# Kernel optimization log

Hardware: AMD Instinct MI355X
Metric: run time of the kernel (lower is better)

Reference implementation:

```python
import jax, jax.numpy as jnp
import numpy as np

KERNEL = 10   # kernel_size (asserted == 10 in the original)
HEADS = 4
BN_SCALE = 1.0 / np.sqrt(1.0 + 1e-5)  # eval-mode BatchNorm1d (running mean 0, var 1, affine 1/0)


def get_dct_matrix(N):
    k = np.arange(N)[:, None].astype(np.float64)
    i = np.arange(N)[None, :].astype(np.float64)
    w = np.full((N, 1), np.sqrt(2.0 / N))
    w[0, 0] = np.sqrt(1.0 / N)
    dct_m = w * np.cos(np.pi * (i + 0.5) * k / N)
    idct_m = np.linalg.inv(dct_m)
    return dct_m.astype(np.float32), idct_m.astype(np.float32)


def conv1d(x, w):  # x [B,C,L], w [O,I,K], valid, no bias
    return jax.lax.conv_general_dilated(x, w, (1,), 'VALID',
                                        dimension_numbers=('NCH', 'OIH', 'NCH'))


def conv_stack(x, w1, w2):  # Conv1d(k=6) -> ReLU -> Conv1d(k=5) -> ReLU
    return jax.nn.relu(conv1d(jax.nn.relu(conv1d(x, w1)), w2))


# vmap over the 4 heads' weights -> [H,B,D,L]
heads_conv = jax.vmap(conv_stack, in_axes=(None, 0, 0))


def _forward(src, cq1, cq2, ck1, ck2, lw, lb, giw, gia, gib, gbw, gba, gbb,
             gow, goa, gob, dct_n, output_n, input_n):
    bs, in_feat = src.shape[0], src.shape[2]
    src = src[:, :input_n]                                   # [B,50,48]
    src_key = jnp.swapaxes(src, 1, 2)[:, :, :input_n - output_n]  # [B,48,25]
    src_query = jnp.swapaxes(src, 1, 2)[:, :, -KERNEL:]           # [B,48,10]

    dct_np, idct_np = get_dct_matrix(KERNEL + output_n)
    dct_m = jnp.asarray(dct_np)
    idct_m = jnp.asarray(idct_np)

    vn = input_n - KERNEL - output_n + 1  # 16 overlapping value windows
    vl = KERNEL + output_n                # window length 35
    idx = np.arange(vl)[None, :] + np.arange(vn)[:, None]    # [16,35]
    windows = src[:, idx]                                    # [B,16,35,48]
    # DCT per window then flatten per-joint coeffs: [B,16,48*dct_n]
    val = jnp.einsum('dv,bnvf->bndf', dct_m[:dct_n], windows)
    src_value = jnp.swapaxes(val, 2, 3).reshape(bs, vn, -1)  # [B,16,480]

    key_h = heads_conv(src_key / 1000.0, ck1, ck2)           # [H,B,512,16]
    query_h = heads_conv(src_query / 1000.0, cq1, cq2)       # [H,B,512,1]

    # sum-normalized (non-softmax) attention
    score = jnp.einsum('hbdq,hbdk->hbqk', query_h, key_h) + 1e-15  # [H,B,1,16]
    att_w = score / jnp.sum(score, axis=3, keepdims=True)
    dct_att = jnp.einsum('hbk,bkf->hbf', att_w[:, :, 0], src_value)  # [H,B,480]
    dct_att = dct_att.reshape(HEADS, bs, in_feat, dct_n)
    att_cat = jnp.transpose(dct_att, (1, 0, 2, 3)).reshape(bs, HEADS * in_feat, dct_n)
    # Linear over the concatenated head/joint axis: [B,48,dct_n]
    att_lin = jnp.einsum('bmd,nm->bnd', att_cat, lw) + lb[None, :, None]

    # last kernel_size frames + last frame repeated output_n times
    gather_idx = np.concatenate([np.arange(input_n - KERNEL, input_n),
                                 np.full(output_n, input_n - 1)])
    input_gcn = src[:, gather_idx]                           # [B,35,48]
    dct_in = jnp.einsum('dv,bvf->bfd', dct_m[:dct_n], input_gcn)  # [B,48,10]
    dct_in = jnp.concatenate([dct_in, att_lin], axis=-1)     # [B,48,20]

    # GCN (Mao et al. style): learnable adjacency [48,48], eval-mode BN, tanh
    def gc(h, a, w, b):
        return jnp.einsum('nm,bmf->bnf', a, h @ w) + b

    y = jnp.tanh(gc(dct_in, gia, giw, gib) * BN_SCALE)       # [B,48,512]
    for s in range(gbw.shape[0]):
        r = y
        for j in range(2):
            y = jnp.tanh(gc(y, gba[s, j], gbw[s, j], gbb[s, j]) * BN_SCALE)
        y = y + r
    dct_out = gc(y, goa, gow, gob) + dct_in                  # [B,48,20]

    out_gcn = jnp.einsum('vd,bnd->bvn', idct_m[:, :dct_n], dct_out[:, :, :dct_n])  # [B,35,48]
    return out_gcn[:, :, None, :]                            # [B,35,itera=1,48]


def setup_inputs() -> dict:
    key = jax.random.key(0)
    ks = jax.random.split(key, 16)
    bs, in_feat, d_model, dct_n = 256, 48, 512, 10
    s = 0.05
    return {
        'src': jax.random.normal(ks[0], (bs, 50, in_feat), jnp.float32) * 1000.0,
        'convQ_w1': jax.random.normal(ks[1], (HEADS, d_model, in_feat, 6), jnp.float32) * s,
        'convQ_w2': jax.random.normal(ks[2], (HEADS, d_model, d_model, 5), jnp.float32) * s,
        'convK_w1': jax.random.normal(ks[3], (HEADS, d_model, in_feat, 6), jnp.float32) * s,
        'convK_w2': jax.random.normal(ks[4], (HEADS, d_model, d_model, 5), jnp.float32) * s,
        'linear_w': jax.random.normal(ks[5], (in_feat, HEADS * in_feat), jnp.float32) * s,
        'linear_b': jax.random.normal(ks[6], (in_feat,), jnp.float32) * s,
        'gc_in_w': jax.random.normal(ks[7], (2 * dct_n, d_model), jnp.float32) * s,
        'gc_in_att': jax.random.normal(ks[8], (in_feat, in_feat), jnp.float32) * s,
        'gc_in_b': jax.random.normal(ks[9], (d_model,), jnp.float32) * s,
        'gcb_w': jax.random.normal(ks[10], (2, 2, d_model, d_model), jnp.float32) * s,
        'gcb_att': jax.random.normal(ks[11], (2, 2, in_feat, in_feat), jnp.float32) * s,
        'gcb_b': jax.random.normal(ks[12], (2, 2, d_model), jnp.float32) * s,
        'gc_out_w': jax.random.normal(ks[13], (d_model, 2 * dct_n), jnp.float32) * s,
        'gc_out_att': jax.random.normal(ks[14], (in_feat, in_feat), jnp.float32) * s,
        'gc_out_b': jax.random.normal(ks[15], (2 * dct_n,), jnp.float32) * s,
        'dct_n': 10, 'output_n': 25, 'input_n': 50, 'itera': 1,
    }


def reference(src, convQ_w1, convQ_w2, convK_w1, convK_w2, linear_w, linear_b,
              gc_in_w, gc_in_att, gc_in_b, gcb_w, gcb_att, gcb_b,
              gc_out_w, gc_out_att, gc_out_b, dct_n, output_n, input_n, itera):
    # itera=1 path only (itera>1 in the original references undefined attrs)
    return _forward(src, convQ_w1, convQ_w2, convK_w1, convK_w2, linear_w, linear_b,
                    gc_in_w, gc_in_att, gc_in_b, gcb_w, gcb_att, gcb_b,
                    gc_out_w, gc_out_att, gc_out_b, dct_n, output_n, input_n)
```

## Files before the change

kernel.cpp:

```cpp
#include <hip/hip_runtime.h>
#include <math.h>

static constexpr float BN_SCALE_F = 0.9999950000374997f;

typedef __bf16 bf16;
typedef bf16 bf16x8 __attribute__((ext_vector_type(8)));
typedef bf16 bf16x4 __attribute__((ext_vector_type(4)));
typedef float floatx4 __attribute__((ext_vector_type(4)));

#define GLOBAL_AS __attribute__((address_space(1)))
#define LDS_AS __attribute__((address_space(3)))

enum { BM_SRC = 0, BM_R1K = 1, BM_PLAIN = 3 };

__device__ __forceinline__ float tanh_fast(float x) {
    const float e = __expf(2.f * x);
    return 1.f - 2.f / (e + 1.f);
}

__device__ __forceinline__ void d_trw1(int id, const float* w, bf16* wt) {
    if (id < 4 * 512 * 320) {
        int ho = id / 320, c = id % 320;
        float v = (c < 288) ? w[(long)ho * 288 + (c % 48) * 6 + (c / 48)] * 1e-3f : 0.f;
        wt[id] = (bf16)v;
    }
}
__global__ __launch_bounds__(256) void k_prep(
    const float* __restrict__ src, const float* __restrict__ cq1,
    const float* __restrict__ ck1, const float* __restrict__ cq2,
    const float* __restrict__ ck2, const float* __restrict__ gbw,
    const float* __restrict__ giw, const float* __restrict__ gow,
    const float* __restrict__ gba, float* __restrict__ dct10,
    bf16* __restrict__ srcbf, bf16* __restrict__ w1tq, bf16* __restrict__ w1tk,
    bf16* __restrict__ w2tq, bf16* __restrict__ w2tk, bf16* __restrict__ gbwF,
    bf16* __restrict__ giwF, bf16* __restrict__ gowT, bf16* __restrict__ gbaP) {
    __shared__ float lds[4160];
    int bb = blockIdx.x;
    const int t = threadIdx.x;
    if (bb < 2) {
        int id = bb * 256 + t;
        if (id < 350) {
            int k = id / 35, i = id % 35;
            double w = (k == 0) ? sqrt(1.0 / 35.0) : sqrt(2.0 / 35.0);
            dct10[id] = (float)(w * cos(3.14159265358979323846 * (i + 0.5) * k / 35.0));
        }
        return;
    }
    bb -= 2;
    if (bb < 2401) {
        int id = bb * 256 + t;
        if (id < 614656) srcbf[id] = (bf16)(id < 614400 ? src[id] : 0.f);
        return;
    }
    bb -= 2401;
    if (bb < 2560) { d_trw1(bb * 256 + t, cq1, w1tq); return; }
    bb -= 2560;
    if (bb < 2560) { d_trw1(bb * 256 + t, ck1, w1tk); return; }
    bb -= 2560;
    if (bb < 4096) {
        const bool isQ = bb < 2048;
        const int ho = isQ ? bb : bb - 2048;
        const float* wrow = (isQ ? cq2 : ck2) + (long)ho * 2560;
        bf16* orow = (isQ ? w2tq : w2tk) + (long)ho * 2560;
        for (int j = t; j < 2560; j += 256) lds[j] = wrow[j];
        __syncthreads();
        for (int c = t; c < 2560; c += 256) {
            const int k = c >> 9, ii = c & 511;
            orow[c] = (bf16)lds[ii * 5 + k];
        }
        return;
    }
    bb -= 4096;
    if (bb < 256) {
        const int l = bb >> 6, tile = bb & 63;
        const int tr = tile >> 3, tc = tile & 7;
        const float* in = gbw + (long)l * 262144;
        bf16* o = gbwF + (long)l * 262144;
#pragma unroll
        for (int r = 0; r < 16; ++r) {
            const int kl = (t >> 6) * 16 + r, ml = t & 63;
            lds[kl * 65 + ml] = in[(long)(tr * 64 + kl) * 512 + tc * 64 + ml];
        }
        __syncthreads();
        for (int j = t; j < 4096; j += 256) {
            const int q = j >> 9, r4 = j & 511;
            const int gl = q >> 2, sl = (q >> 1) & 1, jt = q & 1;
            const int lane = r4 >> 3, e = r4 & 7;
            const int fr = lane & 15, fq = lane >> 4;
            const int kk = sl * 32 + fq * 8 + e;
            const int ff = gl * 32 + jt * 16 + fr;
            o[(long)(tc * 2 + gl) * 16384 + (long)(tr * 2 + sl) * 1024 + jt * 512 + r4] =
                (bf16)lds[kk * 65 + ff];
        }
        return;
    }
    bb -= 256;
    if (bb < 128) {
        int id = bb * 256 + t;
        if (id < 32768) {
            const int r2 = id & 2047;
            const int s = r2 >> 10, r3 = r2 & 1023;
            const int jt = r3 >> 9, r4 = r3 & 511;
            const int lane = r4 >> 3, e = r4 & 7;
            const int fr = lane & 15, fq = lane >> 4;
            const int g = id >> 11;
            const int k = s * 32 + fq * 8 + e;
            const int f = g * 32 + jt * 16 + fr;
            giwF[id] = (bf16)(k < 20 ? giw[k * 512 + f] : 0.f);
        }
        return;
    }
    bb -= 128;
    if (bb < 64) {
        int id = bb * 256 + t;
        int d = id >> 9, k = id & 511;
        gowT[id] = (bf16)(d < 20 ? gow[k * 20 + d] : 0.f);
        return;
    }
    bb -= 64;
    {
        int id = bb * 256 + t;
        if (id < 12288) {
            int l = id / 3072, r = id % 3072, n = r >> 6, m = r & 63;
            gbaP[id] = (bf16)(m < 48 ? gba[l * 2304 + n * 48 + m] : 0.f);
        }
    }
}

struct GP {
    const bf16* A;
    const bf16* B;
    bf16* C;
    int NT;
    int toff;
    int nTiles;
    long aStr, bStr, cStr;
};
template <int BM1, int BM2>
__global__ __launch_bounds__(256) void mgemm2(GP p1, GP p2, const int splitX,
                                              const int M, const int K) {
    const bool first = (int)blockIdx.x < splitX;
    const GP p = first ? p1 : p2;
    const int bx = first ? (int)blockIdx.x : (int)blockIdx.x - splitX;
    if (bx >= p.nTiles) return;
    __shared__ bf16 As[128 * 64];
    __shared__ bf16 Bs[128 * 64];
    const int tid = threadIdx.x;
    const int wave = tid >> 6;
    const int lane = tid & 63;
    const int wm = (wave & 1) << 6;
    const int wn = (wave >> 1) << 6;
    const int m0 = blockIdx.y * 128;
    const int n0 = bx * 128;
    const bf16* A = p.A + (long)blockIdx.z * p.aStr;
    const bf16* B = p.B + (long)blockIdx.z * p.bStr;

    const int srow = lane >> 3;
    const int gch = (lane & 7) ^ srow;
    const bf16* aptr[4];
    const bf16* bptr[4];
#pragma unroll
    for (int i = 0; i < 4; ++i) {
        const int ar = wave * 32 + i * 8 + srow;
        aptr[i] = A + (long)(m0 + ar) * K + gch * 8;
        const int n = n0 + ar;
        long bbase;
        const bool isSrc = first ? (BM1 == BM_SRC) : (BM2 == BM_SRC);
        if (isSrc)
            bbase = (long)(n / p.NT) * 2400 + (long)((n % p.NT) + p.toff) * 48;
        else
            bbase = (long)n * K;
        bptr[i] = B + bbase + gch * 8;
    }
    const int ldsOff = wave * 32 * 64;

    floatx4 acc[4][4];
#pragma unroll
    for (int j = 0; j < 4; ++j)
#pragma unroll
        for (int i = 0; i < 4; ++i) acc[j][i] = (floatx4){0.f, 0.f, 0.f, 0.f};

    const int fr = lane & 15;
    const int fq = lane >> 4;
    const int fx = lane & 7;

    for (int k0 = 0; k0 < K; k0 += 64) {
#pragma unroll
        for (int i = 0; i < 4; ++i) {
            __builtin_amdgcn_global_load_lds(
                (const GLOBAL_AS void*)(aptr[i] + k0),
                (LDS_AS void*)(As + ldsOff + i * 512), 16, 0, 0);
            __builtin_amdgcn_global_load_lds(
                (const GLOBAL_AS void*)(bptr[i] + k0),
                (LDS_AS void*)(Bs + ldsOff + i * 512), 16, 0, 0);
        }
        __syncthreads();
#pragma unroll
        for (int kk = 0; kk < 2; ++kk) {
            bf16x8 af[4], bfr[4];
#pragma unroll
            for (int im = 0; im < 4; ++im)
                af[im] = *(const bf16x8*)(As + (wm + im * 16 + fr) * 64 +
                                          ((((kk << 2) + fq) ^ fx) << 3));
#pragma unroll
            for (int in = 0; in < 4; ++in)
                bfr[in] = *(const bf16x8*)(Bs + (wn + in * 16 + fr) * 64 +
                                           ((((kk << 2) + fq) ^ fx) << 3));
#pragma unroll
            for (int in = 0; in < 4; ++in)
#pragma unroll
                for (int im = 0; im < 4; ++im)
                    acc[in][im] = __builtin_amdgcn_mfma_f32_16x16x32_bf16(
                        af[im], bfr[in], acc[in][im], 0, 0, 0);
        }
        __syncthreads();
    }
#pragma unroll
    for (int in = 0; in < 4; ++in) {
        const long n = n0 + wn + in * 16 + fr;
#pragma unroll
        for (int im = 0; im < 4; ++im) {
            floatx4 v = acc[in][im];
            const long m = m0 + wm + im * 16 + (fq << 2);
            v.x = fmaxf(v.x, 0.f);
            v.y = fmaxf(v.y, 0.f);
            v.z = fmaxf(v.z, 0.f);
            v.w = fmaxf(v.w, 0.f);
            bf16* C = p.C + (long)blockIdx.z * p.cStr + n * M + m;
            bf16x4 ov;
            ov[0] = (bf16)v.x;
            ov[1] = (bf16)v.y;
            ov[2] = (bf16)v.z;
            ov[3] = (bf16)v.w;
            *(bf16x4*)C = ov;
        }
    }
}

__global__ __launch_bounds__(256) void k_conv2(
    const bf16* __restrict__ w2tk, const bf16* __restrict__ r1k,
    bf16* __restrict__ keyh, const bf16* __restrict__ w2tq,
    const bf16* __restrict__ r1q, bf16* __restrict__ qh) {
    const int K = 2560;
    int bx, by, bz;
    const bf16 *A, *B;
    bf16* C;
    bool r1kMode;
    long aStr, bStr, cStr;
    {
        const int i = blockIdx.x;
        if (i < 1024) {
            const int slot = i & 7;
            bz = slot >> 1;
            const int half = slot & 1;
            const int j = i >> 3;
            bx = half * 16 + (j & 15);
            by = j >> 4;
            A = w2tk; B = r1k; C = keyh; r1kMode = true;
            aStr = 512L * 2560; bStr = 2621440L; cStr = 2097152L;
        } else {
            const int j = i - 1024;
            bz = j >> 4;
            const int r = j & 15;
            bx = r & 1;
            by = r >> 1;
            A = w2tq; B = r1q; C = qh; r1kMode = false;
            aStr = 512L * 2560; bStr = 655360L; cStr = 131072L;
        }
    }
    __shared__ bf16 As[64 * 64];
    __shared__ bf16 Bs[128 * 64];
    const int tid = threadIdx.x;
    const int wave = tid >> 6;
    const int lane = tid & 63;
    const int wm = (wave & 1) * 32;
    const int wn = (wave >> 1) * 64;
    const int m0 = by * 64;
    const int n0 = bx * 128;
    A += (long)bz * aStr;
    B += (long)bz * bStr;

    const int srow = lane >> 3;
    const int gch = (lane & 7) ^ srow;
    const bf16* aptr[2];
    const bf16* bptr[4];
#pragma unroll
    for (int i = 0; i < 2; ++i) {
        const int ar = wave * 16 + i * 8 + srow;
        aptr[i] = A + (long)(m0 + ar) * K + gch * 8;
    }
#pragma unroll
    for (int i = 0; i < 4; ++i) {
        const int ar = wave * 32 + i * 8 + srow;
        const int n = n0 + ar;
        const long bbase = r1kMode ? (long)((n >> 4) * 20 + (n & 15)) * 512
                                   : (long)n * K;
        bptr[i] = B + bbase + gch * 8;
    }

    floatx4 acc[4][2];
#pragma unroll
    for (int j = 0; j < 4; ++j)
#pragma unroll
        for (int i = 0; i < 2; ++i) acc[j][i] = (floatx4){0.f, 0.f, 0.f, 0.f};

    const int fr = lane & 15;
    const int fq = lane >> 4;
    const int fx = lane & 7;

    for (int k0 = 0; k0 < K; k0 += 64) {
#pragma unroll
        for (int i = 0; i < 2; ++i)
            __builtin_amdgcn_global_load_lds(
                (const GLOBAL_AS void*)(aptr[i] + k0),
                (LDS_AS void*)(As + (wave * 16 + i * 8) * 64), 16, 0, 0);
#pragma unroll
        for (int i = 0; i < 4; ++i)
            __builtin_amdgcn_global_load_lds(
                (const GLOBAL_AS void*)(bptr[i] + k0),
                (LDS_AS void*)(Bs + (wave * 32 + i * 8) * 64), 16, 0, 0);
        __syncthreads();
#pragma unroll
        for (int kk = 0; kk < 2; ++kk) {
            bf16x8 af[2], bfr[4];
#pragma unroll
            for (int im = 0; im < 2; ++im)
                af[im] = *(const bf16x8*)(As + (wm + im * 16 + fr) * 64 +
                                          ((((kk << 2) + fq) ^ fx) << 3));
#pragma unroll
            for (int in = 0; in < 4; ++in)
                bfr[in] = *(const bf16x8*)(Bs + (wn + in * 16 + fr) * 64 +
                                           ((((kk << 2) + fq) ^ fx) << 3));
#pragma unroll
            for (int in = 0; in < 4; ++in)
#pragma unroll
                for (int im = 0; im < 2; ++im)
                    acc[in][im] = __builtin_amdgcn_mfma_f32_16x16x32_bf16(
                        af[im], bfr[in], acc[in][im], 0, 0, 0);
        }
        __syncthreads();
    }
#pragma unroll
    for (int in = 0; in < 4; ++in) {
        const long n = n0 + wn + in * 16 + fr;
#pragma unroll
        for (int im = 0; im < 2; ++im) {
            floatx4 v = acc[in][im];
            const long m = m0 + wm + im * 16 + (fq << 2);
            v.x = fmaxf(v.x, 0.f);
            v.y = fmaxf(v.y, 0.f);
            v.z = fmaxf(v.z, 0.f);
            v.w = fmaxf(v.w, 0.f);
            bf16* Cp = C + (long)bz * cStr + n * 512 + m;
            bf16x4 ov;
            ov[0] = (bf16)v.x;
            ov[1] = (bf16)v.y;
            ov[2] = (bf16)v.z;
            ov[3] = (bf16)v.w;
            *(bf16x4*)Cp = ov;
        }
    }
}

__global__ __launch_bounds__(512) void k_att(
    const bf16* __restrict__ qh, const bf16* __restrict__ keyh,
    const float* __restrict__ src, const float* __restrict__ dct10,
    const float* __restrict__ lw, const float* __restrict__ lb,
    const float* __restrict__ gia, float* __restrict__ dctin,
    bf16* __restrict__ z0) {
    const int b = blockIdx.x;
    const int t = threadIdx.x;
    __shared__ float BIG[9216];
    __shared__ float WD[2400];
    __shared__ float D[350];
    __shared__ float L[1920];
    __shared__ float dinS[960];
    __shared__ float sS[64];
    __shared__ float awS[64];

    {
        const int g = t >> 3, lane = t & 7;
        const int h = g >> 4, tt = g & 15;
        const bf16* q = qh + ((long)h * 256 + b) * 512 + lane * 64;
        const bf16* kr = keyh + (long)h * 2097152 + ((long)b * 16 + tt) * 512 + lane * 64;
        float p = 0.f;
#pragma unroll
        for (int i = 0; i < 8; ++i) {
            const bf16x8 qv = *(const bf16x8*)(q + i * 8);
            const bf16x8 kv = *(const bf16x8*)(kr + i * 8);
#pragma unroll
            for (int j = 0; j < 8; ++j) p = fmaf((float)qv[j], (float)kv[j], p);
        }
        p += __shfl_down(p, 4, 8);
        p += __shfl_down(p, 2, 8);
        p += __shfl_down(p, 1, 8);
        if (lane == 0) sS[g] = p + 1e-15f;
    }
    for (int i = t; i < 2400; i += 512) WD[i] = src[(long)b * 2400 + i];
    for (int i = t; i < 350; i += 512) D[i] = dct10[i];
    __syncthreads();
    if (t < 4) {
        float s = 0.f;
#pragma unroll
        for (int k = 0; k < 16; ++k) s += sS[t * 16 + k];
        const float inv = 1.f / s;
#pragma unroll
        for (int k = 0; k < 16; ++k) awS[t * 16 + k] = sS[t * 16 + k] * inv;
    }
    __syncthreads();
    if (t < 480) {
        const int f = t / 10, d = t % 10;
        float dreg[35];
#pragma unroll
        for (int v = 0; v < 35; ++v) dreg[v] = D[d * 35 + v];
#pragma unroll 2
        for (int n = 0; n < 16; ++n) {
            float acc = 0.f;
#pragma unroll
            for (int v = 0; v < 35; ++v)
                acc = fmaf(dreg[v], WD[(n + v) * 48 + f], acc);
            BIG[n * 480 + t] = acc;
        }
        float acc = 0.f;
#pragma unroll
        for (int v = 0; v < 10; ++v)
            acc = fmaf(dreg[v], WD[(40 + v) * 48 + f], acc);
        float cs = 0.f;
#pragma unroll
        for (int v = 10; v < 35; ++v) cs += dreg[v];
        acc = fmaf(cs, WD[49 * 48 + f], acc);
        dinS[f * 20 + d] = acc;
        dctin[(long)b * 960 + f * 20 + d] = acc;
    }
    __syncthreads();
    for (int p = 0; p < 4; ++p) {
        const int idx = t + p * 512;
        if (idx < 1920) {
            const int h = idx / 480, j = idx % 480;
            float acc = 0.f;
#pragma unroll
            for (int k = 0; k < 16; ++k)
                acc = fmaf(awS[h * 16 + k], BIG[k * 480 + j], acc);
            L[idx] = acc;
        }
    }
    __syncthreads();
    for (int i = t; i < 9216; i += 512) BIG[i] = lw[i];
    for (int i = t; i < 2304; i += 512) WD[i] = gia[i];
    __syncthreads();
    if (t < 480) {
        const int n = t / 10, d = t % 10;
        float acc = lb[n];
#pragma unroll
        for (int h = 0; h < 4; ++h)
#pragma unroll
            for (int f = 0; f < 48; ++f)
                acc = fmaf(BIG[n * 192 + h * 48 + f], L[h * 480 + f * 10 + d], acc);
        dinS[n * 20 + 10 + d] = acc;
        dctin[(long)b * 960 + n * 20 + 10 + d] = acc;
    }
    __syncthreads();
    for (int p = 0; p < 2; ++p) {
        const int idx = t + p * 512;
        if (idx < 960) {
            const int n = idx / 20, d = idx % 20;
            float acc = 0.f;
#pragma unroll
            for (int m = 0; m < 48; ++m)
                acc = fmaf(WD[n * 48 + m], dinS[m * 20 + d], acc);
            z0[((long)b * 48 + n) * 64 + d] = (bf16)acc;
        }
    }
    for (int i = t; i < 2112; i += 512) {
        const int n = i / 44, c = 20 + i % 44;
        z0[((long)b * 48 + n) * 64 + c] = (bf16)0.f;
    }
}

template <bool TOUT, int S>
__device__ __forceinline__ void gcn_matmul3(
    const bf16* __restrict__ zSrc, const bf16* __restrict__ Wf,
    const float* __restrict__ bias, const bf16* __restrict__ resT,
    bf16* __restrict__ outS, const int wave, const int lane) {
    const int fr = lane & 15, fq = lane >> 4;
    const int f0 = wave * 32;
    floatx4 acc[3][2];
#pragma unroll
    for (int it = 0; it < 3; ++it)
#pragma unroll
        for (int jt = 0; jt < 2; ++jt) acc[it][jt] = (floatx4){0.f, 0.f, 0.f, 0.f};
    const bf16* wp = Wf + (long)wave * (S * 1024) + (lane << 3);
    bf16x8 w0[4], w1[4];
    constexpr int PRE = (S < 3) ? S : 3;
#pragma unroll
    for (int s = 0; s < PRE; ++s) {
        w0[s] = *(const bf16x8*)(wp + s * 1024);
        w1[s] = *(const bf16x8*)(wp + s * 1024 + 512);
    }
#pragma unroll
    for (int s = 0; s < S; ++s) {
        bf16x8 af[3];
#pragma unroll
        for (int it = 0; it < 3; ++it)
            af[it] = *(const bf16x8*)(zSrc + (it * 16 + fr) * 520 + s * 32 + fq * 8);
        if (s + 3 < S) {
            const int ns = (s + 3) & 3;
            w0[ns] = *(const bf16x8*)(wp + (s + 3) * 1024);
            w1[ns] = *(const bf16x8*)(wp + (s + 3) * 1024 + 512);
        }
        const int sl = s & 3;
#pragma unroll
        for (int it = 0; it < 3; ++it) {
            acc[it][0] = __builtin_amdgcn_mfma_f32_16x16x32_bf16(af[it], w0[sl],
                                                                acc[it][0], 0, 0, 0);
            acc[it][1] = __builtin_amdgcn_mfma_f32_16x16x32_bf16(af[it], w1[sl],
                                                                acc[it][1], 0, 0, 0);
        }
    }
#pragma unroll
    for (int jt = 0; jt < 2; ++jt) {
        const int f = f0 + jt * 16 + fr;
        const float bv = bias[f];
#pragma unroll
        for (int it = 0; it < 3; ++it) {
            const int ir0 = it * 16 + fq * 4;
            float v[4];
#pragma unroll
            for (int r = 0; r < 4; ++r)
                v[r] = tanh_fast((acc[it][jt][r] + bv) * BN_SCALE_F);
            if (resT) {
                const bf16x4 rv = *(const bf16x4*)(resT + f * 48 + ir0);
#pragma unroll
                for (int r = 0; r < 4; ++r) v[r] += (float)rv[r];
            }
            if (TOUT) {
                bf16x4 ov;
#pragma unroll
                for (int r = 0; r < 4; ++r) ov[r] = (bf16)v[r];
                *(bf16x4*)(outS + f * 48 + ir0) = ov;
            } else {
#pragma unroll
                for (int r = 0; r < 4; ++r)
                    outS[(ir0 + r) * 520 + f] = (bf16)v[r];
            }
        }
    }
}

__device__ __forceinline__ void gcn_attmul2(const bf16* __restrict__ gA,
                                            const bf16* __restrict__ YinT,
                                            bf16* __restrict__ zOut,
                                            const int wave, const int lane) {
    const int fr = lane & 15, fq = lane >> 4;
    const int f0 = wave * 32;
    floatx4 acc[3][2];
#pragma unroll
    for (int it = 0; it < 3; ++it)
#pragma unroll
        for (int jt = 0; jt < 2; ++jt) acc[it][jt] = (floatx4){0.f, 0.f, 0.f, 0.f};
    bf16x8 af0[3], af1[3], bv0[2], bv1[2];
#pragma unroll
    for (int it = 0; it < 3; ++it) {
        af0[it] = *(const bf16x8*)(gA + (it * 16 + fr) * 64 + fq * 8);
        af1[it] = *(const bf16x8*)(gA + (it * 16 + fr) * 64 + 32 + fq * 8);
    }
#pragma unroll
    for (int jt = 0; jt < 2; ++jt) {
        const int f = f0 + jt * 16 + fr;
        bv0[jt] = *(const bf16x8*)(YinT + f * 48 + fq * 8);
        bv1[jt] = *(const bf16x8*)(YinT + f * 48 + 32 + fq * 8);
    }
#pragma unroll
    for (int it = 0; it < 3; ++it)
#pragma unroll
        for (int jt = 0; jt < 2; ++jt) {
            acc[it][jt] = __builtin_amdgcn_mfma_f32_16x16x32_bf16(af0[it], bv0[jt],
                                                                 acc[it][jt], 0, 0, 0);
            acc[it][jt] = __builtin_amdgcn_mfma_f32_16x16x32_bf16(af1[it], bv1[jt],
                                                                 acc[it][jt], 0, 0, 0);
        }
#pragma unroll
    for (int jt = 0; jt < 2; ++jt) {
        const int f = f0 + jt * 16 + fr;
#pragma unroll
        for (int it = 0; it < 3; ++it)
#pragma unroll
            for (int r = 0; r < 4; ++r)
                zOut[(it * 16 + fq * 4 + r) * 520 + f] = (bf16)acc[it][jt][r];
    }
}

__global__ __launch_bounds__(1024) void k_gcn(
    const bf16* __restrict__ z0, const bf16* __restrict__ giwF,
    const float* __restrict__ gib, const bf16* __restrict__ gbwF,
    const bf16* __restrict__ gbaP, const float* __restrict__ gbb,
    const float* __restrict__ goa, const bf16* __restrict__ gowT,
    const float* __restrict__ gob, const float* __restrict__ dctin,
    const float* __restrict__ dct10, float* __restrict__ out) {
    const int b = blockIdx.x;
    const int t = threadIdx.x;
    const int wave = t >> 6, lane = t & 63;
    __shared__ __align__(16) bf16 yaS[24976];
    __shared__ __align__(16) bf16 ybS[24592];
    __shared__ __align__(16) bf16 zS[48 * 520];

    if (t < 384) {
        const int r = t >> 3, c = t & 7;
        *(bf16x8*)(zS + r * 520 + c * 8) =
            *(const bf16x8*)(z0 + ((long)b * 48 + r) * 64 + c * 8);
    } else if (t < 400) {
        yaS[24576 + (t - 384)] = (bf16)0.f;
    } else if (t < 416) {
        ybS[24576 + (t - 400)] = (bf16)0.f;
    }
    __syncthreads();
    gcn_matmul3<true, 2>(zS, giwF, gib, nullptr, yaS, wave, lane);
    __syncthreads();

#pragma unroll
    for (int l = 0; l < 4; ++l) {
        const bf16* YinT = (l == 0 || l == 3) ? yaS : ybS;
        gcn_attmul2(gbaP + l * 3072, YinT, zS, wave, lane);
        __syncthreads();
        const bf16* Res = (l == 1) ? yaS : (l == 3 ? ybS : nullptr);
        if (l < 3)
            gcn_matmul3<true, 16>(zS, gbwF + (long)l * 262144, gbb + l * 512,
                                  Res, (l < 2) ? ybS : yaS, wave, lane);
        else
            gcn_matmul3<false, 16>(zS, gbwF + 3L * 262144, gbb + 3 * 512, Res,
                                   yaS, wave, lane);
        __syncthreads();
    }
    float* T2 = (float*)ybS;
    float* dS = ((float*)ybS) + 960;
    float* goaS = ((float*)ybS) + 1920;
    float* Df = ((float*)ybS) + 4224;
    if (t < 384) {
        const int fr2 = lane & 15, fq2 = lane >> 4;
        const int it = wave >> 1, jt = wave & 1;
        floatx4 accT = (floatx4){0.f, 0.f, 0.f, 0.f};
        const bf16* ap = yaS + (it * 16 + fr2) * 520 + fq2 * 8;
        const bf16* gp = gowT + (long)(jt * 16 + fr2) * 512 + fq2 * 8;
        for (int k0 = 0; k0 < 512; k0 += 32) {
            const bf16x8 av = *(const bf16x8*)(ap + k0);
            const bf16x8 gv = *(const bf16x8*)(gp + k0);
            accT = __builtin_amdgcn_mfma_f32_16x16x32_bf16(av, gv, accT, 0, 0, 0);
        }
        const int d = jt * 16 + fr2;
        if (d < 20) {
#pragma unroll
            for (int r = 0; r < 4; ++r) {
                const int m = it * 16 + fq2 * 4 + r;
                T2[m * 20 + d] = accT[r];
            }
        }
    } else {
        for (int i = t - 384; i < 2304; i += 640) goaS[i] = goa[i];
        for (int i = t - 384; i < 350; i += 640) Df[i] = dct10[i];
    }
    __syncthreads();
    if (t < 960) {
        const int n = t / 20, d = t % 20;
        float acc = gob[d] + dctin[(long)b * 960 + t];
#pragma unroll
        for (int m = 0; m < 48; ++m)
            acc = fmaf(goaS[n * 48 + m], T2[m * 20 + d], acc);
        dS[t] = acc;
    }
    __syncthreads();
    for (int e = t; e < 1680; e += 1024) {
        const int v = e / 48, n = e % 48;
        float acc = 0.f;
#pragma unroll
        for (int d = 0; d < 10; ++d)
            acc = fmaf(Df[d * 35 + v], dS[n * 20 + d], acc);
        out[(long)b * 1680 + e] = acc;
    }
}

static constexpr size_t WS_DCT10 = 0;
static constexpr size_t WS_ATTW = 1536;
static constexpr size_t WS_QH = WS_ATTW + 65536;
static constexpr size_t WS_DCTIN = WS_QH + 2097152;
static constexpr size_t WS_DCTOUT = WS_DCTIN + 983040;
static constexpr size_t WS_SRCVAL = WS_DCTOUT + 983040;
static constexpr size_t WS_PAD0 = WS_SRCVAL + 7864320;
static constexpr size_t WS_GOWT = WS_PAD0;
static constexpr size_t WS_GBAP = WS_PAD0 + 32768;
static constexpr size_t WS_SRCBF = WS_PAD0 + 8388608;
static constexpr size_t WS_W1TQ = WS_SRCBF + 1229824;
static constexpr size_t WS_W1TK = WS_W1TQ + 1310720;
static constexpr size_t WS_W2TQ = WS_W1TK + 1310720;
static constexpr size_t WS_W2TK = WS_W2TQ + 10485760;
static constexpr size_t WS_GBWT = WS_W2TK + 10485760;
static constexpr size_t WS_R1K = WS_GBWT + 2097152;
static constexpr size_t WS_R1Q = WS_R1K + 20971520;
static constexpr size_t WS_T = WS_R1Q + 5242880;
static constexpr size_t WS_GIWP = WS_T + 50331648;
static constexpr size_t WS_KEYH = WS_T;
static constexpr size_t WS_Z0 = WS_T + 17825792;

extern "C" void kernel_launch(void* const* d_in, const int* in_sizes, int n_in,
                              void* d_out, int out_size, void* d_ws,
                              size_t ws_size, hipStream_t stream) {
    const float* src = (const float*)d_in[0];
    const float* cq1 = (const float*)d_in[1];
    const float* cq2 = (const float*)d_in[2];
    const float* ck1 = (const float*)d_in[3];
    const float* ck2 = (const float*)d_in[4];
    const float* lw = (const float*)d_in[5];
    const float* lb = (const float*)d_in[6];
    const float* giw = (const float*)d_in[7];
    const float* gia = (const float*)d_in[8];
    const float* gib = (const float*)d_in[9];
    const float* gbw = (const float*)d_in[10];
    const float* gba = (const float*)d_in[11];
    const float* gbb = (const float*)d_in[12];
    const float* gow = (const float*)d_in[13];
    const float* goa = (const float*)d_in[14];
    const float* gob = (const float*)d_in[15];
    float* out = (float*)d_out;
    char* ws = (char*)d_ws;

    float* dct10 = (float*)(ws + WS_DCT10);
    bf16* qh = (bf16*)(ws + WS_QH);
    float* dctin = (float*)(ws + WS_DCTIN);
    bf16* keyh = (bf16*)(ws + WS_KEYH);
    bf16* srcbf = (bf16*)(ws + WS_SRCBF);
    bf16* w1tq = (bf16*)(ws + WS_W1TQ);
    bf16* w1tk = (bf16*)(ws + WS_W1TK);
    bf16* w2tq = (bf16*)(ws + WS_W2TQ);
    bf16* w2tk = (bf16*)(ws + WS_W2TK);
    bf16* gbwF = (bf16*)(ws + WS_GBWT);
    bf16* r1k = (bf16*)(ws + WS_R1K);
    bf16* r1q = (bf16*)(ws + WS_R1Q);
    bf16* giwF = (bf16*)(ws + WS_GIWP);
    bf16* gowT = (bf16*)(ws + WS_GOWT);
    bf16* gbaP = (bf16*)(ws + WS_GBAP);
    bf16* z0 = (bf16*)(ws + WS_Z0);

    k_prep<<<12115, 256, 0, stream>>>(src, cq1, ck1, cq2, ck2, gbw, giw, gow,
                                      gba, dct10, srcbf, w1tq, w1tk, w2tq,
                                      w2tk, gbwF, giwF, gowT, gbaP);

    {
        GP pk{w1tk, srcbf, r1k, 20, 0, 40, 512L * 320, 0L, 5120L * 512};
        GP pq{w1tq, srcbf, r1q, 5, 40, 10, 512L * 320, 0L, 1280L * 512};
        mgemm2<BM_SRC, BM_SRC><<<dim3(56, 4, 4), 256, 0, stream>>>(pk, pq, 40,
                                                                   512, 320);
    }
    k_conv2<<<1088, 256, 0, stream>>>(w2tk, r1k, keyh, w2tq, r1q, qh);

    k_att<<<256, 512, 0, stream>>>(qh, keyh, src, dct10, lw, lb, gia, dctin, z0);

    k_gcn<<<256, 1024, 0, stream>>>(z0, giwF, gib, gbwF, gbaP, gbb, goa, gowT,
                                    gob, dctin, dct10, out);
}
```

Before: 306.0 us.

## Pre-pack conv2 weights into MFMA fragment order and load A directly to registers

The prep kernel now writes the second conv weights in a fragment-major layout that matches the MFMA A-operand lane order. k_conv2 then reads A fragments straight from global memory into registers, with no LDS staging, and keeps only B in LDS. The wave tiling changes so each wave covers all 64 M rows and 32 N columns. This drops the A LDS traffic and its shared-memory footprint, in exchange for more register pressure and uncoalesced-latency exposure on global A loads.

```diff
diff --git a/kernel.cpp b/kernel.cpp
--- a/kernel.cpp
+++ b/kernel.cpp
@@ -32,9 +32,9 @@
     const float* __restrict__ giw, const float* __restrict__ gow,
     const float* __restrict__ gba, float* __restrict__ dct10,
     bf16* __restrict__ srcbf, bf16* __restrict__ w1tq, bf16* __restrict__ w1tk,
-    bf16* __restrict__ w2tq, bf16* __restrict__ w2tk, bf16* __restrict__ gbwF,
+    bf16* __restrict__ w2qF, bf16* __restrict__ w2kF, bf16* __restrict__ gbwF,
     bf16* __restrict__ giwF, bf16* __restrict__ gowT, bf16* __restrict__ gbaP) {
-    __shared__ float lds[4160];
+    __shared__ float lds[10240];
     int bb = blockIdx.x;
     const int t = threadIdx.x;
     if (bb < 2) {
@@ -57,20 +57,29 @@
     bb -= 2560;
     if (bb < 2560) { d_trw1(bb * 256 + t, ck1, w1tk); return; }
     bb -= 2560;
-    if (bb < 4096) {
-        const bool isQ = bb < 2048;
-        const int ho = isQ ? bb : bb - 2048;
-        const float* wrow = (isQ ? cq2 : ck2) + (long)ho * 2560;
-        bf16* orow = (isQ ? w2tq : w2tk) + (long)ho * 2560;
-        for (int j = t; j < 2560; j += 256) lds[j] = wrow[j];
+    if (bb < 1024) {
+        const bool isQ = bb < 512;
+        const int rb = isQ ? bb : bb - 512;
+        const float* W = isQ ? cq2 : ck2;
+        bf16* o = isQ ? w2qF : w2kF;
+        const int r0 = rb * 4;
+        const int z = r0 >> 9, row = r0 & 511;
+        const int g = row >> 5, im = (row >> 4) & 1, fr0 = row & 15;
+        const float* wr = W + (long)r0 * 2560;
+        for (int j = t; j < 10240; j += 256) lds[j] = wr[j];
         __syncthreads();
-        for (int c = t; c < 2560; c += 256) {
-            const int k = c >> 9, ii = c & 511;
-            orow[c] = (bf16)lds[ii * 5 + k];
+        bf16* ob = o + ((long)(z * 16 + g) * 40) * 2048;
+        for (int j = t; j < 10240; j += 256) {
+            const int e = j & 7, rr = (j >> 3) & 3, fq = (j >> 5) & 3;
+            const int kk = (j >> 7) & 1, s = j >> 8;
+            const int k = s * 64 + kk * 32 + fq * 8 + e;
+            const int m = k & 511, w = k >> 9;
+            ob[(long)s * 2048 + kk * 1024 + im * 512 + fq * 128 + (fr0 + rr) * 8 + e] =
+                (bf16)lds[rr * 2560 + m * 5 + w];
         }
         return;
     }
-    bb -= 4096;
+    bb -= 1024;
     if (bb < 256) {
         const int l = bb >> 6, tile = bb & 63;
         const int tr = tile >> 3, tc = tile & 7;
@@ -238,15 +247,15 @@
 }
 
 __global__ __launch_bounds__(256) void k_conv2(
-    const bf16* __restrict__ w2tk, const bf16* __restrict__ r1k,
-    bf16* __restrict__ keyh, const bf16* __restrict__ w2tq,
+    const bf16* __restrict__ w2kF, const bf16* __restrict__ r1k,
+    bf16* __restrict__ keyh, const bf16* __restrict__ w2qF,
     const bf16* __restrict__ r1q, bf16* __restrict__ qh) {
-    const int K = 2560;
+    const int NT = 40;
     int bx, by, bz;
-    const bf16 *A, *B;
+    const bf16 *AF, *B;
     bf16* C;
-    bool r1kMode;
-    long aStr, bStr, cStr;
+    bool kMode;
+    long bStr, cStr;
     {
         const int i = blockIdx.x;
         if (i < 1024) {
@@ -256,97 +265,88 @@
             const int j = i >> 3;
             bx = half * 16 + (j & 15);
             by = j >> 4;
-            A = w2tk; B = r1k; C = keyh; r1kMode = true;
-            aStr = 512L * 2560; bStr = 2621440L; cStr = 2097152L;
+            AF = w2kF; B = r1k; C = keyh; kMode = true;
+            bStr = 2621440L; cStr = 2097152L;
         } else {
             const int j = i - 1024;
             bz = j >> 4;
             const int r = j & 15;
             bx = r & 1;
             by = r >> 1;
-            A = w2tq; B = r1q; C = qh; r1kMode = false;
-            aStr = 512L * 2560; bStr = 655360L; cStr = 131072L;
-        }
-    }
-    __shared__ bf16 As[64 * 64];
+            AF = w2qF; B = r1q; C = qh; kMode = false;
+            bStr = 655360L; cStr = 131072L;
+        }
+    }
     __shared__ bf16 Bs[128 * 64];
     const int tid = threadIdx.x;
     const int wave = tid >> 6;
     const int lane = tid & 63;
-    const int wm = (wave & 1) * 32;
-    const int wn = (wave >> 1) * 64;
+    const int wn = wave * 32;
     const int m0 = by * 64;
     const int n0 = bx * 128;
-    A += (long)bz * aStr;
     B += (long)bz * bStr;
 
     const int srow = lane >> 3;
     const int gch = (lane & 7) ^ srow;
-    const bf16* aptr[2];
     const bf16* bptr[4];
-#pragma unroll
-    for (int i = 0; i < 2; ++i) {
-        const int ar = wave * 16 + i * 8 + srow;
-        aptr[i] = A + (long)(m0 + ar) * K + gch * 8;
-    }
 #pragma unroll
     for (int i = 0; i < 4; ++i) {
         const int ar = wave * 32 + i * 8 + srow;
         const int n = n0 + ar;
-        const long bbase = r1kMode ? (long)((n >> 4) * 20 + (n & 15)) * 512
-                                   : (long)n * K;
+        const long bbase = kMode ? (long)((n >> 4) * 20 + (n & 15)) * 512
+                                 : (long)n * 2560;
         bptr[i] = B + bbase + gch * 8;
     }
+    const bf16* ap = AF + ((long)(bz * 16 + by * 2) * 40) * 2048 + lane * 8;
 
     floatx4 acc[4][2];
 #pragma unroll
-    for (int j = 0; j < 4; ++j)
-#pragma unroll
-        for (int i = 0; i < 2; ++i) acc[j][i] = (floatx4){0.f, 0.f, 0.f, 0.f};
+    for (int mt = 0; mt < 4; ++mt)
+#pragma unroll
+        for (int nt = 0; nt < 2; ++nt) acc[mt][nt] = (floatx4){0.f, 0.f, 0.f, 0.f};
 
     const int fr = lane & 15;
     const int fq = lane >> 4;
     const int fx = lane & 7;
 
-    for (int k0 = 0; k0 < K; k0 += 64) {
-#pragma unroll
-        for (int i = 0; i < 2; ++i)
-            __builtin_amdgcn_global_load_lds(
-                (const GLOBAL_AS void*)(aptr[i] + k0),
-                (LDS_AS void*)(As + (wave * 16 + i * 8) * 64), 16, 0, 0);
+    for (int s = 0; s < NT; ++s) {
 #pragma unroll
         for (int i = 0; i < 4; ++i)
             __builtin_amdgcn_global_load_lds(
-                (const GLOBAL_AS void*)(bptr[i] + k0),
+                (const GLOBAL_AS void*)(bptr[i] + s * 64),
                 (LDS_AS void*)(Bs + (wave * 32 + i * 8) * 64), 16, 0, 0);
+        bf16x8 a[2][4];
+#pragma unroll
+        for (int kk = 0; kk < 2; ++kk)
+#pragma unroll
+            for (int mt = 0; mt < 4; ++mt)
+                a[kk][mt] = *(const bf16x8*)(ap + (long)(mt >> 1) * 81920 +
+                                             (long)s * 2048 + kk * 1024 +
+                                             (mt & 1) * 512);
         __syncthreads();
 #pragma unroll
         for (int kk = 0; kk < 2; ++kk) {
-            bf16x8 af[2], bfr[4];
-#pragma unroll
-            for (int im = 0; im < 2; ++im)
-                af[im] = *(const bf16x8*)(As + (wm + im * 16 + fr) * 64 +
-                                          ((((kk << 2) + fq) ^ fx) << 3));
-#pragma unroll
-            for (int in = 0; in < 4; ++in)
-                bfr[in] = *(const bf16x8*)(Bs + (wn + in * 16 + fr) * 64 +
+            bf16x8 bfr[2];
+#pragma unroll
+            for (int nt = 0; nt < 2; ++nt)
+                bfr[nt] = *(const bf16x8*)(Bs + (wn + nt * 16 + fr) * 64 +
                                            ((((kk << 2) + fq) ^ fx) << 3));
 #pragma unroll
-            for (int in = 0; in < 4; ++in)
-#pragma unroll
-                for (int im = 0; im < 2; ++im)
-                    acc[in][im] = __builtin_amdgcn_mfma_f32_16x16x32_bf16(
-                        af[im], bfr[in], acc[in][im], 0, 0, 0);
+            for (int mt = 0; mt < 4; ++mt)
+#pragma unroll
+                for (int nt = 0; nt < 2; ++nt)
+                    acc[mt][nt] = __builtin_amdgcn_mfma_f32_16x16x32_bf16(
+                        a[kk][mt], bfr[nt], acc[mt][nt], 0, 0, 0);
         }
         __syncthreads();
     }
 #pragma unroll
-    for (int in = 0; in < 4; ++in) {
-        const long n = n0 + wn + in * 16 + fr;
-#pragma unroll
-        for (int im = 0; im < 2; ++im) {
-            floatx4 v = acc[in][im];
-            const long m = m0 + wm + im * 16 + (fq << 2);
+    for (int nt = 0; nt < 2; ++nt) {
+        const long n = n0 + wn + nt * 16 + fr;
+#pragma unroll
+        for (int mt = 0; mt < 4; ++mt) {
+            floatx4 v = acc[mt][nt];
+            const long m = m0 + mt * 16 + (fq << 2);
             v.x = fmaxf(v.x, 0.f);
             v.y = fmaxf(v.y, 0.f);
             v.z = fmaxf(v.z, 0.f);
@@ -729,8 +729,8 @@
     bf16* srcbf = (bf16*)(ws + WS_SRCBF);
     bf16* w1tq = (bf16*)(ws + WS_W1TQ);
     bf16* w1tk = (bf16*)(ws + WS_W1TK);
-    bf16* w2tq = (bf16*)(ws + WS_W2TQ);
-    bf16* w2tk = (bf16*)(ws + WS_W2TK);
+    bf16* w2qF = (bf16*)(ws + WS_W2TQ);
+    bf16* w2kF = (bf16*)(ws + WS_W2TK);
     bf16* gbwF = (bf16*)(ws + WS_GBWT);
     bf16* r1k = (bf16*)(ws + WS_R1K);
     bf16* r1q = (bf16*)(ws + WS_R1Q);
@@ -739,9 +739,9 @@
     bf16* gbaP = (bf16*)(ws + WS_GBAP);
     bf16* z0 = (bf16*)(ws + WS_Z0);
 
-    k_prep<<<12115, 256, 0, stream>>>(src, cq1, ck1, cq2, ck2, gbw, giw, gow,
-                                      gba, dct10, srcbf, w1tq, w1tk, w2tq,
-                                      w2tk, gbwF, giwF, gowT, gbaP);
+    k_prep<<<9043, 256, 0, stream>>>(src, cq1, ck1, cq2, ck2, gbw, giw, gow,
+                                     gba, dct10, srcbf, w1tq, w1tk, w2qF,
+                                     w2kF, gbwF, giwF, gowT, gbaP);
 
     {
         GP pk{w1tk, srcbf, r1k, 20, 0, 40, 512L * 320, 0L, 5120L * 512};
@@ -749,7 +749,7 @@
         mgemm2<BM_SRC, BM_SRC><<<dim3(56, 4, 4), 256, 0, stream>>>(pk, pq, 40,
                                                                    512, 320);
     }
-    k_conv2<<<1088, 256, 0, stream>>>(w2tk, r1k, keyh, w2tq, r1q, qh);
+    k_conv2<<<1088, 256, 0, stream>>>(w2kF, r1k, keyh, w2qF, r1q, qh);
 
     k_att<<<256, 512, 0, stream>>>(qh, keyh, src, dct10, lw, lb, gia, dctin, z0);
 
```

After: 332.0 us. +8.5%, slower.
